# Kernel tuning notes

Measured on AMD Instinct MI355X. Metric: run time of the kernel, lower is better.

The kernel has to match this reference:

```python
import jax, jax.numpy as jnp
import numpy as np

N_NODES = 100000
N_EDGES = 1600000
HIDDEN = 64
LEAKY_SLOPE = 0.01  # torch F.leaky_relu default


def setup_inputs() -> dict:
    key = jax.random.key(0)
    k1, k2, k3, k4 = jax.random.split(key, 4)
    x = jax.random.normal(k1, (N_NODES, HIDDEN), dtype=jnp.float32)
    edge_index = jax.random.randint(k2, (2, N_EDGES), 0, N_NODES, dtype=jnp.int64)
    # Linear(hidden, 1, bias=False) weights, squeezed to [hidden]
    w_i = jax.random.normal(k3, (HIDDEN,), dtype=jnp.float32) * 0.1
    w_j = jax.random.normal(k4, (HIDDEN,), dtype=jnp.float32) * 0.1
    return {"x": x, "edge_index": edge_index, "w_i": w_i, "w_j": w_j}


def reference(x, edge_index, w_i, w_j):
    n = x.shape[0]
    ej, ei = edge_index[0], edge_index[1]  # (edge_index_j, edge_index_i)
    # per-node attention scores, then per-edge gather
    s_i = x @ w_i  # [N]
    s_j = x @ w_j  # [N]
    e = jax.nn.leaky_relu(s_i[ei] + s_j[ej], LEAKY_SLOPE)  # [E]
    # segment softmax over edges grouped by destination node ei
    emax = jax.ops.segment_max(e, ei, num_segments=n)  # [N]
    ex = jnp.exp(e - emax[ei])  # [E]
    denom = jax.ops.segment_sum(ex, ei, num_segments=n)  # [N]
    alpha = ex / denom[ei]  # [E]
    # spmm: out[i] = sum_{edges e: dst=i} alpha_e * x[src_e]
    out = jax.ops.segment_sum(alpha[:, None] * x[ej], ei, num_segments=n)  # [N, H]
    return jax.nn.relu(out)
```

## Files before the change

### kernel.cpp

```cpp
#include <hip/hip_runtime.h>
#include <stdint.h>

#define N_NODES 100000
#define N_EDGES 1600000
#define HIDDEN  64
#define SLOPE   0.01f
#define NBUCK   782
#define CAPB    2816
#define PCHUNK  4096
#define NPART   391
#define CAP     1024

__device__ __forceinline__ unsigned short f2bf(float f) {
    uint32_t u = __float_as_uint(f);
    uint32_t r = u + 0x7FFFu + ((u >> 16) & 1u);
    return (unsigned short)(r >> 16);
}

__global__ void __launch_bounds__(256) k_scores(const float* __restrict__ x,
                                                const float* __restrict__ w_i,
                                                const float* __restrict__ w_j,
                                                float* __restrict__ s_i,
                                                float* __restrict__ s_j,
                                                unsigned short* __restrict__ xb) {
    int tid = threadIdx.x;
    int node = blockIdx.x * 4 + (tid >> 6);
    int lane = tid & 63;
    if (node >= N_NODES) return;
    float v = x[node * HIDDEN + lane];
    xb[node * HIDDEN + lane] = f2bf(v);
    float a = v * w_i[lane];
    float b = v * w_j[lane];
    for (int off = 32; off > 0; off >>= 1) {
        a += __shfl_xor(a, off, 64);
        b += __shfl_xor(b, off, 64);
    }
    if (lane == 0) { s_i[node] = a; s_j[node] = b; }
}

__global__ void __launch_bounds__(1024) k_partition(const int* __restrict__ srcs,
                                                    const int* __restrict__ dsts,
                                                    int* __restrict__ cursor,
                                                    uint32_t* __restrict__ pairs) {
    __shared__ int lcnt[NBUCK], lbase[NBUCK];
    int tid = threadIdx.x;
    if (tid < NBUCK) lcnt[tid] = 0;
    __syncthreads();
    int e0 = blockIdx.x * PCHUNK;
    int e1 = min(e0 + PCHUNK, N_EDGES);
    for (int e = e0 + tid; e < e1; e += 1024)
        atomicAdd(&lcnt[dsts[e] >> 7], 1);
    __syncthreads();
    if (tid < NBUCK) {
        int c = lcnt[tid];
        lbase[tid] = c ? atomicAdd(&cursor[tid], c) : 0;
        lcnt[tid] = 0;
    }
    __syncthreads();
    for (int e = e0 + tid; e < e1; e += 1024) {
        int src = srcs[e];
        int dst = dsts[e];
        int b = dst >> 7;
        int r = atomicAdd(&lcnt[b], 1);
        int pos = lbase[b] + r;
        if (pos < CAPB)
            pairs[(size_t)b * CAPB + pos] =
                ((uint32_t)(dst & 127) << 24) | (uint32_t)src;
    }
}

__device__ __forceinline__ float bflo(uint32_t d) { return __uint_as_float(d << 16); }
__device__ __forceinline__ float bfhi(uint32_t d) { return __uint_as_float(d & 0xFFFF0000u); }

template <int L>
__device__ __forceinline__ void gat_batch(const uint64_t* pp, int i, int half, int hl,
                                          const uint32_t* __restrict__ xw,
                                          float& accL, float& accH, float& den) {
    uint64_t q[L];
    uint32_t d[L];
#pragma unroll
    for (int t = 0; t < L; ++t) q[t] = pp[i + 2 * t + half];
#pragma unroll
    for (int t = 0; t < L; ++t)
        d[t] = xw[((uint32_t)q[t] & 0xFFFFFFu) * 32 + hl];
#pragma unroll
    for (int t = 0; t < L; ++t) {
        float w = __uint_as_float((uint32_t)(q[t] >> 32));
        den += w;
        accL = fmaf(w, bflo(d[t]), accL);
        accH = fmaf(w, bfhi(d[t]), accH);
    }
}

__global__ void __launch_bounds__(256, 8) k_bucket_agg(const uint32_t* __restrict__ xw,
                                                       const uint32_t* __restrict__ pairs,
                                                       const int* __restrict__ cursor,
                                                       const float* __restrict__ s_i,
                                                       const float* __restrict__ s_j,
                                                       float* __restrict__ out) {
    __shared__ uint64_t spairs[CAP];
    __shared__ int scnt[32], soff[32], scnt2[32];
    __shared__ float s_si[32];
    __shared__ int sovf;
    int tid = threadIdx.x;
    int g = blockIdx.x;
    int cb = g >> 2, sub = g & 3;
    int node0 = g * 32;
    const uint32_t* reg = pairs + (size_t)cb * CAPB;
    int rcnt = min(cursor[cb], CAPB);
    if (tid < 32) {
        scnt[tid] = 0; scnt2[tid] = 0;
        int node = node0 + tid;
        s_si[tid] = (node < N_NODES) ? s_i[node] : 0.f;
    }
    if (tid == 0) sovf = 0;
    __syncthreads();
    for (int e = tid; e < rcnt; e += 256) {
        int dstl = (int)(reg[e] >> 24);
        if ((dstl >> 5) == sub) atomicAdd(&scnt[dstl & 31], 1);
    }
    __syncthreads();
    if (tid < 32) {
        int v = scnt[tid], s = v;
        for (int o = 1; o < 32; o <<= 1) {
            int t = __shfl_up(s, o, 64);
            if (tid >= o) s += t;
        }
        soff[tid] = s - v;
        if (tid == 31 && s > CAP) sovf = 1;
    }
    __syncthreads();
    int ovf = sovf;
    if (!ovf) {
        for (int e = tid; e < rcnt; e += 256) {
            uint32_t p = reg[e];
            int dstl = (int)(p >> 24);
            if ((dstl >> 5) == sub) {
                int n = dstl & 31;
                int src = (int)(p & 0xFFFFFFu);
                float sc = s_si[n] + s_j[src];
                sc = (sc > 0.f) ? sc : SLOPE * sc;
                float w = __expf(sc);
                int r = atomicAdd(&scnt2[n], 1);
                spairs[soff[n] + r] =
                    ((uint64_t)__float_as_uint(w) << 32) | (uint32_t)src;
            }
        }
    }
    __syncthreads();
    int wave = tid >> 6, lane = tid & 63;
    int half = lane >> 5, hl = lane & 31;
    for (int k = wave; k < 32; k += 4) {
        int node = node0 + k;
        if (node >= N_NODES) break;
        float accL = 0.f, accH = 0.f, den = 0.f;
        int c = scnt[k];
        if (!ovf) {
            const uint64_t* pp = spairs + soff[k];
            int i = 0;
            for (; i + 16 <= c; i += 16) gat_batch<8>(pp, i, half, hl, xw, accL, accH, den);
            if (i + 8 <= c) { gat_batch<4>(pp, i, half, hl, xw, accL, accH, den); i += 8; }
            if (i + 4 <= c) { gat_batch<2>(pp, i, half, hl, xw, accL, accH, den); i += 4; }
            if (i + 2 <= c) { gat_batch<1>(pp, i, half, hl, xw, accL, accH, den); i += 2; }
            if (i < c) {
                uint64_t q = pp[i];
                float w = half ? 0.f : __uint_as_float((uint32_t)(q >> 32));
                uint32_t d = xw[((uint32_t)q & 0xFFFFFFu) * 32 + hl];
                den += w;
                accL = fmaf(w, bflo(d), accL);
                accH = fmaf(w, bfhi(d), accH);
            }
        } else {
            int sn = (sub << 5) | k;
            for (int e = 0; e < rcnt; ++e) {
                uint32_t p = reg[e];
                if ((int)(p >> 24) == sn) {
                    int src = (int)(p & 0xFFFFFFu);
                    float sc = s_si[k] + s_j[src];
                    sc = (sc > 0.f) ? sc : SLOPE * sc;
                    float w = half ? 0.f : __expf(sc);
                    uint32_t d = xw[(uint32_t)src * 32 + hl];
                    den += w;
                    accL = fmaf(w, bflo(d), accL);
                    accH = fmaf(w, bfhi(d), accH);
                }
            }
        }
        accL += __shfl_xor(accL, 32, 64);
        accH += __shfl_xor(accH, 32, 64);
        den  += __shfl_xor(den, 32, 64);
        if (half == 0) {
            float rL = 0.f, rH = 0.f;
            if (c > 0) {
                float inv = 1.f / den;
                rL = fmaxf(accL * inv, 0.f);
                rH = fmaxf(accH * inv, 0.f);
            }
            ((float2*)(out + (size_t)node * HIDDEN))[hl] = make_float2(rL, rH);
        }
    }
}

extern "C" void kernel_launch(void* const* d_in, const int* in_sizes, int n_in,
                              void* d_out, int out_size, void* d_ws, size_t ws_size,
                              hipStream_t stream) {
    const float* x   = (const float*)d_in[0];
    const int*   ei  = (const int*)d_in[1];
    const float* w_i = (const float*)d_in[2];
    const float* w_j = (const float*)d_in[3];
    float* out = (float*)d_out;

    char* p = (char*)d_ws;
    float*          s_i    = (float*)p;          p += (size_t)N_NODES * 4;
    float*          s_j    = (float*)p;          p += (size_t)N_NODES * 4;
    unsigned short* xb     = (unsigned short*)p; p += (size_t)N_NODES * HIDDEN * 2;
    int*            cursor = (int*)p;            p += 4096;
    uint32_t*       pairs  = (uint32_t*)p;

    const int* srcs = ei;
    const int* dsts = ei + N_EDGES;

    hipMemsetAsync(cursor, 0, NBUCK * sizeof(int), stream);
    k_scores    <<<(N_NODES + 3) / 4, 256, 0, stream>>>(x, w_i, w_j, s_i, s_j, xb);
    k_partition <<<NPART, 1024, 0, stream>>>(srcs, dsts, cursor, pairs);
    k_bucket_agg<<<(N_NODES + 31) / 32, 256, 0, stream>>>((const uint32_t*)xb, pairs, cursor, s_i, s_j, out);
}
```

Before: 168.4 us.

## Fuse score and partition kernels; gather 8-byte bf16 rows with quarter-wave split

Result: slower. 176.4 us (+4.7%).

```diff
diff --git a/kernel.cpp b/kernel.cpp
--- a/kernel.cpp
+++ b/kernel.cpp
@@ -9,6 +9,7 @@
 #define CAPB    2816
 #define PCHUNK  4096
 #define NPART   391
+#define NSB     25000
 #define CAP     1024
 
 __device__ __forceinline__ unsigned short f2bf(float f) {
@@ -17,47 +18,48 @@
     return (unsigned short)(r >> 16);
 }
 
-__global__ void __launch_bounds__(256) k_scores(const float* __restrict__ x,
-                                                const float* __restrict__ w_i,
-                                                const float* __restrict__ w_j,
-                                                float* __restrict__ s_i,
-                                                float* __restrict__ s_j,
-                                                unsigned short* __restrict__ xb) {
-    int tid = threadIdx.x;
-    int node = blockIdx.x * 4 + (tid >> 6);
-    int lane = tid & 63;
-    if (node >= N_NODES) return;
-    float v = x[node * HIDDEN + lane];
-    xb[node * HIDDEN + lane] = f2bf(v);
-    float a = v * w_i[lane];
-    float b = v * w_j[lane];
-    for (int off = 32; off > 0; off >>= 1) {
-        a += __shfl_xor(a, off, 64);
-        b += __shfl_xor(b, off, 64);
-    }
-    if (lane == 0) { s_i[node] = a; s_j[node] = b; }
-}
-
-__global__ void __launch_bounds__(1024) k_partition(const int* __restrict__ srcs,
-                                                    const int* __restrict__ dsts,
-                                                    int* __restrict__ cursor,
-                                                    uint32_t* __restrict__ pairs) {
+__global__ void __launch_bounds__(256) k_build(const float* __restrict__ x,
+                                               const float* __restrict__ w_i,
+                                               const float* __restrict__ w_j,
+                                               const int* __restrict__ srcs,
+                                               const int* __restrict__ dsts,
+                                               float* __restrict__ s_i,
+                                               float* __restrict__ s_j,
+                                               unsigned short* __restrict__ xb,
+                                               int* __restrict__ cursor,
+                                               uint32_t* __restrict__ pairs) {
     __shared__ int lcnt[NBUCK], lbase[NBUCK];
     int tid = threadIdx.x;
-    if (tid < NBUCK) lcnt[tid] = 0;
-    __syncthreads();
-    int e0 = blockIdx.x * PCHUNK;
+    if (blockIdx.x < NSB) {
+        int node = blockIdx.x * 4 + (tid >> 6);
+        int lane = tid & 63;
+        if (node >= N_NODES) return;
+        float v = x[node * HIDDEN + lane];
+        xb[node * HIDDEN + lane] = f2bf(v);
+        float a = v * w_i[lane];
+        float b = v * w_j[lane];
+        for (int off = 32; off > 0; off >>= 1) {
+            a += __shfl_xor(a, off, 64);
+            b += __shfl_xor(b, off, 64);
+        }
+        if (lane == 0) { s_i[node] = a; s_j[node] = b; }
+        return;
+    }
+    int pb = blockIdx.x - NSB;
+    for (int b = tid; b < NBUCK; b += 256) lcnt[b] = 0;
+    __syncthreads();
+    int e0 = pb * PCHUNK;
     int e1 = min(e0 + PCHUNK, N_EDGES);
-    for (int e = e0 + tid; e < e1; e += 1024)
+    for (int e = e0 + tid; e < e1; e += 256)
         atomicAdd(&lcnt[dsts[e] >> 7], 1);
     __syncthreads();
-    if (tid < NBUCK) {
-        int c = lcnt[tid];
-        lbase[tid] = c ? atomicAdd(&cursor[tid], c) : 0;
-        lcnt[tid] = 0;
-    }
-    __syncthreads();
-    for (int e = e0 + tid; e < e1; e += 1024) {
+    for (int b = tid; b < NBUCK; b += 256) {
+        int c = lcnt[b];
+        lbase[b] = c ? atomicAdd(&cursor[b], c) : 0;
+        lcnt[b] = 0;
+    }
+    __syncthreads();
+    for (int e = e0 + tid; e < e1; e += 256) {
         int src = srcs[e];
         int dst = dsts[e];
         int b = dst >> 7;
@@ -73,26 +75,28 @@
 __device__ __forceinline__ float bfhi(uint32_t d) { return __uint_as_float(d & 0xFFFF0000u); }
 
 template <int L>
-__device__ __forceinline__ void gat_batch(const uint64_t* pp, int i, int half, int hl,
-                                          const uint32_t* __restrict__ xw,
-                                          float& accL, float& accH, float& den) {
+__device__ __forceinline__ void gat_batch4(const uint64_t* pp, int i, int quarter, int ql,
+                                           const uint2* __restrict__ xw2,
+                                           float acc[4], float& den) {
     uint64_t q[L];
-    uint32_t d[L];
-#pragma unroll
-    for (int t = 0; t < L; ++t) q[t] = pp[i + 2 * t + half];
+    uint2 d[L];
+#pragma unroll
+    for (int t = 0; t < L; ++t) q[t] = pp[i + 4 * t + quarter];
 #pragma unroll
     for (int t = 0; t < L; ++t)
-        d[t] = xw[((uint32_t)q[t] & 0xFFFFFFu) * 32 + hl];
+        d[t] = xw2[((uint32_t)q[t] & 0xFFFFFFu) * 16 + ql];
 #pragma unroll
     for (int t = 0; t < L; ++t) {
         float w = __uint_as_float((uint32_t)(q[t] >> 32));
         den += w;
-        accL = fmaf(w, bflo(d[t]), accL);
-        accH = fmaf(w, bfhi(d[t]), accH);
-    }
-}
-
-__global__ void __launch_bounds__(256, 8) k_bucket_agg(const uint32_t* __restrict__ xw,
+        acc[0] = fmaf(w, bflo(d[t].x), acc[0]);
+        acc[1] = fmaf(w, bfhi(d[t].x), acc[1]);
+        acc[2] = fmaf(w, bflo(d[t].y), acc[2]);
+        acc[3] = fmaf(w, bfhi(d[t].y), acc[3]);
+    }
+}
+
+__global__ void __launch_bounds__(256, 8) k_bucket_agg(const uint2* __restrict__ xw2,
                                                        const uint32_t* __restrict__ pairs,
                                                        const int* __restrict__ cursor,
                                                        const float* __restrict__ s_i,
@@ -149,26 +153,29 @@
     }
     __syncthreads();
     int wave = tid >> 6, lane = tid & 63;
-    int half = lane >> 5, hl = lane & 31;
+    int quarter = lane >> 4, ql = lane & 15;
     for (int k = wave; k < 32; k += 4) {
         int node = node0 + k;
         if (node >= N_NODES) break;
-        float accL = 0.f, accH = 0.f, den = 0.f;
+        float acc[4] = {0.f, 0.f, 0.f, 0.f};
+        float den = 0.f;
         int c = scnt[k];
         if (!ovf) {
             const uint64_t* pp = spairs + soff[k];
             int i = 0;
-            for (; i + 16 <= c; i += 16) gat_batch<8>(pp, i, half, hl, xw, accL, accH, den);
-            if (i + 8 <= c) { gat_batch<4>(pp, i, half, hl, xw, accL, accH, den); i += 8; }
-            if (i + 4 <= c) { gat_batch<2>(pp, i, half, hl, xw, accL, accH, den); i += 4; }
-            if (i + 2 <= c) { gat_batch<1>(pp, i, half, hl, xw, accL, accH, den); i += 2; }
-            if (i < c) {
-                uint64_t q = pp[i];
-                float w = half ? 0.f : __uint_as_float((uint32_t)(q >> 32));
-                uint32_t d = xw[((uint32_t)q & 0xFFFFFFu) * 32 + hl];
+            for (; i + 16 <= c; i += 16) gat_batch4<4>(pp, i, quarter, ql, xw2, acc, den);
+            if (i + 8 <= c) { gat_batch4<2>(pp, i, quarter, ql, xw2, acc, den); i += 8; }
+            if (i + 4 <= c) { gat_batch4<1>(pp, i, quarter, ql, xw2, acc, den); i += 4; }
+            int rem = c - i;
+            if (rem > 0) {
+                uint64_t q = pp[i + min(quarter, rem - 1)];
+                float w = (quarter < rem) ? __uint_as_float((uint32_t)(q >> 32)) : 0.f;
+                uint2 d = xw2[((uint32_t)q & 0xFFFFFFu) * 16 + ql];
                 den += w;
-                accL = fmaf(w, bflo(d), accL);
-                accH = fmaf(w, bfhi(d), accH);
+                acc[0] = fmaf(w, bflo(d.x), acc[0]);
+                acc[1] = fmaf(w, bfhi(d.x), acc[1]);
+                acc[2] = fmaf(w, bflo(d.y), acc[2]);
+                acc[3] = fmaf(w, bfhi(d.y), acc[3]);
             }
         } else {
             int sn = (sub << 5) | k;
@@ -178,25 +185,33 @@
                     int src = (int)(p & 0xFFFFFFu);
                     float sc = s_si[k] + s_j[src];
                     sc = (sc > 0.f) ? sc : SLOPE * sc;
-                    float w = half ? 0.f : __expf(sc);
-                    uint32_t d = xw[(uint32_t)src * 32 + hl];
+                    float w = (quarter == 0) ? __expf(sc) : 0.f;
+                    uint2 d = xw2[(uint32_t)src * 16 + ql];
                     den += w;
-                    accL = fmaf(w, bflo(d), accL);
-                    accH = fmaf(w, bfhi(d), accH);
+                    acc[0] = fmaf(w, bflo(d.x), acc[0]);
+                    acc[1] = fmaf(w, bfhi(d.x), acc[1]);
+                    acc[2] = fmaf(w, bflo(d.y), acc[2]);
+                    acc[3] = fmaf(w, bfhi(d.y), acc[3]);
                 }
             }
         }
-        accL += __shfl_xor(accL, 32, 64);
-        accH += __shfl_xor(accH, 32, 64);
-        den  += __shfl_xor(den, 32, 64);
-        if (half == 0) {
-            float rL = 0.f, rH = 0.f;
+#pragma unroll
+        for (int j = 0; j < 4; ++j) {
+            acc[j] += __shfl_xor(acc[j], 16, 64);
+            acc[j] += __shfl_xor(acc[j], 32, 64);
+        }
+        den += __shfl_xor(den, 16, 64);
+        den += __shfl_xor(den, 32, 64);
+        if (quarter == 0) {
+            float4 r = make_float4(0.f, 0.f, 0.f, 0.f);
             if (c > 0) {
                 float inv = 1.f / den;
-                rL = fmaxf(accL * inv, 0.f);
-                rH = fmaxf(accH * inv, 0.f);
-            }
-            ((float2*)(out + (size_t)node * HIDDEN))[hl] = make_float2(rL, rH);
+                r.x = fmaxf(acc[0] * inv, 0.f);
+                r.y = fmaxf(acc[1] * inv, 0.f);
+                r.z = fmaxf(acc[2] * inv, 0.f);
+                r.w = fmaxf(acc[3] * inv, 0.f);
+            }
+            ((float4*)(out + (size_t)node * HIDDEN))[ql] = r;
         }
     }
 }
@@ -221,7 +236,8 @@
     const int* dsts = ei + N_EDGES;
 
     hipMemsetAsync(cursor, 0, NBUCK * sizeof(int), stream);
-    k_scores    <<<(N_NODES + 3) / 4, 256, 0, stream>>>(x, w_i, w_j, s_i, s_j, xb);
-    k_partition <<<NPART, 1024, 0, stream>>>(srcs, dsts, cursor, pairs);
-    k_bucket_agg<<<(N_NODES + 31) / 32, 256, 0, stream>>>((const uint32_t*)xb, pairs, cursor, s_i, s_j, out);
-}
+    k_build     <<<NSB + NPART, 256, 0, stream>>>(x, w_i, w_j, srcs, dsts,
+                                                  s_i, s_j, xb, cursor, pairs);
+    k_bucket_agg<<<(N_NODES + 31) / 32, 256, 0, stream>>>((const uint2*)xb, pairs, cursor,
+                                                          s_i, s_j, out);
+}
```
